# Kernel tuning notes

Measured on AMD Instinct MI355X. Metric: run time of the kernel, lower is better.

Reference implementation:

```python
import jax, jax.numpy as jnp
import numpy as np

B, Q, K, H, DV = 16, 256, 256, 256, 256


def setup_inputs() -> dict:
    key = jax.random.key(0)
    ks = jax.random.split(key, 6)
    return {
        "queries": jax.random.normal(ks[0], (B, Q, H), dtype=jnp.float32),
        "keys": jax.random.normal(ks[1], (B, K, H), dtype=jnp.float32),
        "values": jax.random.normal(ks[2], (B, K, DV), dtype=jnp.float32),
        "W_q": jax.random.normal(ks[3], (H, H), dtype=jnp.float32) / np.sqrt(H),
        "W_k": jax.random.normal(ks[4], (H, H), dtype=jnp.float32) / np.sqrt(H),
        "w_v": jax.random.normal(ks[5], (H,), dtype=jnp.float32) / np.sqrt(H),
    }


def reference(queries, keys, values, W_q, W_k, w_v):
    # Linear projections (nn.Linear: x @ W.T), bias-free
    q = jnp.einsum("bqd,hd->bqh", queries, W_q)  # [B,Q,H]
    k = jnp.einsum("bkd,hd->bkh", keys, W_k)      # [B,K,H]
    # Broadcast add -> tanh -> scalar projection
    features = jnp.tanh(q[:, :, None, :] + k[:, None, :, :])  # [B,Q,K,H]
    scores = jnp.einsum("bqkh,h->bqk", features, w_v)          # [B,Q,K]
    attn = jax.nn.softmax(scores, axis=-1)                      # [B,Q,K]
    return jnp.einsum("bqk,bkv->bqv", attn, values)            # [B,Q,DV]
```

## Files before the change

### kernel.cpp

```cpp
#include <hip/hip_runtime.h>

#define Bn 16
#define Qn 256
#define Kn 256
#define Hn 256
#define DVn 256

constexpr float C2    = 2.8853900817779268f;
constexpr float LOG2E = 1.4426950408889634f;

typedef __attribute__((ext_vector_type(8))) short bf16x8;
typedef __attribute__((ext_vector_type(4))) float f32x4;

__device__ __forceinline__ float fast_exp2(float x) { return __builtin_amdgcn_exp2f(x); }
__device__ __forceinline__ float fast_rcp(float x)  { return __builtin_amdgcn_rcpf(x); }

__device__ __forceinline__ unsigned short f2bf(float x) {
    unsigned u = __float_as_uint(x);
    u += 0x7fffu + ((u >> 16) & 1u);
    return (unsigned short)(u >> 16);
}

__device__ __forceinline__ bf16x8 cvt8(const float* p) {
    float4 x0 = *(const float4*)p;
    float4 x1 = *(const float4*)(p + 4);
    bf16x8 r;
    r[0] = (short)f2bf(x0.x); r[1] = (short)f2bf(x0.y);
    r[2] = (short)f2bf(x0.z); r[3] = (short)f2bf(x0.w);
    r[4] = (short)f2bf(x1.x); r[5] = (short)f2bf(x1.y);
    r[6] = (short)f2bf(x1.z); r[7] = (short)f2bf(x1.w);
    return r;
}

__global__ __launch_bounds__(256)
void proj_mfma_kernel(const float* __restrict__ q, const float* __restrict__ kx,
                      const float* __restrict__ wq, const float* __restrict__ wk,
                      const float* __restrict__ V,
                      float* __restrict__ Eq, unsigned short* __restrict__ Ekb,
                      float* __restrict__ Vp)
{
    const int tid  = threadIdx.x;
    const int wvid = tid >> 6, lane = tid & 63;
    const int bid  = blockIdx.x;
    const int m0   = (bid >> 1) * 16;
    const int n0   = (bid & 1) * 128 + wvid * 32;
    const bool isQ = (m0 < 4096);
    const int r16  = lane & 15, q8 = (lane >> 4) * 8;

    const float* Xrow = (isQ ? q + (size_t)(m0 + r16) * 256
                             : kx + (size_t)(m0 - 4096 + r16) * 256) + q8;
    bf16x8 afr[8];
    #pragma unroll
    for (int s = 0; s < 8; ++s) afr[s] = cvt8(Xrow + s * 32);

    const float* Wbase = isQ ? wq : wk;
    f32x4 acc[2];
    #pragma unroll
    for (int nt = 0; nt < 2; ++nt) {
        const float* Wrow = Wbase + (size_t)(n0 + nt * 16 + r16) * 256 + q8;
        f32x4 c = {0.f, 0.f, 0.f, 0.f};
        #pragma unroll
        for (int s = 0; s < 8; ++s) {
            bf16x8 bfr = cvt8(Wrow + s * 32);
            c = __builtin_amdgcn_mfma_f32_16x16x32_bf16(afr[s], bfr, c, 0, 0, 0);
        }
        acc[nt] = c;
    }
    const int rbase = (lane >> 4) * 4;
    #pragma unroll
    for (int nt = 0; nt < 2; ++nt) {
        const int n = n0 + nt * 16 + r16;
        #pragma unroll
        for (int r = 0; r < 4; ++r) {
            const int m = m0 + rbase + r;
            const float val = fast_exp2(C2 * acc[nt][r]);
            if (isQ) {
                Eq[(size_t)m * 256 + n] = val;
            } else {
                const int kr = m - 4096, b = kr >> 8, kk = kr & 255;
                Ekb[(((size_t)(b * 64 + (n >> 2))) * 256 + kk) * 4 + (n & 3)] = f2bf(val);
            }
        }
    }
    {
        const int p   = bid * 256 + tid;
        const int bk4 = p >> 8, dv = p & 255;
        const int b   = bk4 >> 6, k4 = bk4 & 63;
        const float* src = V + ((size_t)(b * Kn + 4 * k4)) * DVn + dv;
        float4 o;
        o.x = src[0 * DVn]; o.y = src[1 * DVn]; o.z = src[2 * DVn]; o.w = src[3 * DVn];
        *(float4*)(Vp + (size_t)p * 4) = o;
    }
}

__global__ __launch_bounds__(512, 8)
void fused_attn_kernel(const float* __restrict__ Eq, const unsigned short* __restrict__ Ekb,
                       const float* __restrict__ wv, const float* __restrict__ Vp,
                       float* __restrict__ out)
{
    const int b    = blockIdx.y;
    const int q0   = blockIdx.x * 4;
    const int tid  = threadIdx.x;
    const int kk   = tid & 255;
    const int half = tid >> 8;
    const int halfu = __builtin_amdgcn_readfirstlane(half);

    __shared__ __align__(16) float sPart[2][256][4];
    __shared__ __align__(16) float sPv[256 * 4];
    __shared__ float sredM[4][8];
    __shared__ float sredS[4][8];

    const float* eq0 = Eq + (size_t)(b * Qn + q0) * Hn + halfu * 128;
    const float* wv0 = wv + halfu * 128;

    float sc[4] = {0.f, 0.f, 0.f, 0.f};
    const uint2* ekp = (const uint2*)Ekb + (size_t)b * 16384 + (size_t)(halfu * 32) * 256 + kk;
    uint2 e[4];
    #pragma unroll
    for (int g = 0; g < 4; ++g) e[g] = ekp[g * 256];
    for (int it = 0; it < 8; ++it) {
        uint2 en[4];
        if (it < 7) {
            #pragma unroll
            for (int g = 0; g < 4; ++g) en[g] = ekp[(4 * (it + 1) + g) * 256];
        }
        const int h0 = it * 16;
        float ek[16];
        #pragma unroll
        for (int g = 0; g < 4; ++g) {
            ek[4*g+0] = __uint_as_float(e[g].x << 16);
            ek[4*g+1] = __uint_as_float(e[g].x & 0xFFFF0000u);
            ek[4*g+2] = __uint_as_float(e[g].y << 16);
            ek[4*g+3] = __uint_as_float(e[g].y & 0xFFFF0000u);
        }
        #pragma unroll
        for (int g = 0; g < 4; ++g) {
            const float4 wa = *(const float4*)(wv0 + h0 + 4 * g);
            #pragma unroll
            for (int qq = 0; qq < 4; ++qq) {
                const float4 ea = *(const float4*)(eq0 + qq * 256 + h0 + 4 * g);
                float a = sc[qq];
                a = fmaf(wa.x, fast_rcp(fmaf(ea.x, ek[4*g+0], 1.f)), a);
                a = fmaf(wa.y, fast_rcp(fmaf(ea.y, ek[4*g+1], 1.f)), a);
                a = fmaf(wa.z, fast_rcp(fmaf(ea.z, ek[4*g+2], 1.f)), a);
                a = fmaf(wa.w, fast_rcp(fmaf(ea.w, ek[4*g+3], 1.f)), a);
                sc[qq] = a;
            }
        }
        #pragma unroll
        for (int g = 0; g < 4; ++g) e[g] = en[g];
    }

    *(float4*)&sPart[half][kk][0] = make_float4(sc[0], sc[1], sc[2], sc[3]);
    __syncthreads();
    const float4 pa = *(const float4*)&sPart[0][kk][0];
    const float4 pb = *(const float4*)&sPart[1][kk][0];
    float tot[4] = {pa.x + pb.x, pa.y + pb.y, pa.z + pb.z, pa.w + pb.w};

    const int w = tid >> 6, lane = tid & 63;
    #pragma unroll
    for (int qq = 0; qq < 4; ++qq) {
        tot[qq] = -2.0f * tot[qq];
        float mx = tot[qq];
        #pragma unroll
        for (int off = 32; off; off >>= 1) mx = fmaxf(mx, __shfl_xor(mx, off, 64));
        if (lane == 0) sredM[qq][w] = mx;
    }
    __syncthreads();
    float pq[4];
    #pragma unroll
    for (int qq = 0; qq < 4; ++qq) {
        float mx = sredM[qq][0];
        #pragma unroll
        for (int i = 1; i < 8; ++i) mx = fmaxf(mx, sredM[qq][i]);
        pq[qq] = fast_exp2(LOG2E * (tot[qq] - mx));
        float s = pq[qq];
        #pragma unroll
        for (int off = 32; off; off >>= 1) s += __shfl_xor(s, off, 64);
        if (lane == 0) sredS[qq][w] = s;
    }
    if (halfu == 0) *(float4*)&sPv[kk * 4] = make_float4(pq[0], pq[1], pq[2], pq[3]);
    __syncthreads();
    float rinv[4];
    #pragma unroll
    for (int qq = 0; qq < 4; ++qq) {
        float s = sredS[qq][0];
        #pragma unroll
        for (int i = 1; i < 8; ++i) s += sredS[qq][i];
        rinv[qq] = fast_rcp(0.5f * s);
    }

    float acc[4] = {0.f, 0.f, 0.f, 0.f};
    const float4* vp = (const float4*)Vp + (size_t)b * 64 * 256 + (size_t)(halfu * 32) * 256 + kk;
    float4 vv = vp[0];
    for (int k4 = 0; k4 < 32; ++k4) {
        float4 vn;
        if (k4 < 31) vn = vp[(k4 + 1) * 256];
        const int kb = (halfu * 32 + k4) * 4;
        const float vj[4] = {vv.x, vv.y, vv.z, vv.w};
        #pragma unroll
        for (int j = 0; j < 4; ++j) {
            const float4 p4 = *(const float4*)&sPv[(kb + j) * 4];
            acc[0] = fmaf(p4.x, vj[j], acc[0]);
            acc[1] = fmaf(p4.y, vj[j], acc[1]);
            acc[2] = fmaf(p4.z, vj[j], acc[2]);
            acc[3] = fmaf(p4.w, vj[j], acc[3]);
        }
        vv = vn;
    }
    *(float4*)&sPart[half][kk][0] = make_float4(acc[0], acc[1], acc[2], acc[3]);
    __syncthreads();
    {
        const int dv = kk;
        const float4 u0 = *(const float4*)&sPart[0][dv][0];
        const float4 u1 = *(const float4*)&sPart[1][dv][0];
        float a0, a1;
        if (halfu == 0) { a0 = u0.x + u1.x; a1 = u0.y + u1.y; }
        else            { a0 = u0.z + u1.z; a1 = u0.w + u1.w; }
        float* ob = out + (size_t)(b * Qn + q0 + 2 * halfu) * DVn + dv;
        ob[0]   = a0 * rinv[2 * halfu + 0];
        ob[DVn] = a1 * rinv[2 * halfu + 1];
    }
}

extern "C" void kernel_launch(void* const* d_in, const int* in_sizes, int n_in,
                              void* d_out, int out_size, void* d_ws, size_t ws_size,
                              hipStream_t stream) {
    const float* queries = (const float*)d_in[0];
    const float* keys    = (const float*)d_in[1];
    const float* values  = (const float*)d_in[2];
    const float* W_q     = (const float*)d_in[3];
    const float* W_k     = (const float*)d_in[4];
    const float* w_v     = (const float*)d_in[5];
    float* out = (float*)d_out;

    float*          Eq  = (float*)d_ws;
    unsigned short* Ekb = (unsigned short*)(Eq + (size_t)Bn * Qn * Hn);
    float*          Vp  = (float*)(Ekb + (size_t)Bn * Kn * Hn);

    proj_mfma_kernel<<<dim3(1024), 256, 0, stream>>>(queries, keys, W_q, W_k, values,
                                                     Eq, Ekb, Vp);
    fused_attn_kernel<<<dim3(64, 16), 512, 0, stream>>>(Eq, Ekb, w_v, Vp, out);
}
```

Before: 132.8 us.

## Pre-convert inputs and weights to bf16 in separate prep kernel before MFMA projection

Adds a prep kernel that converts queries, keys and both weight matrices to bf16 once and also performs the V repacking. The projection kernel then loads bf16 fragments directly and each block covers all 256 output columns (4 waves x 64), halving the grid. This removes the repeated fp32-to-bf16 conversion of the weight rows in every block and halves how often the X rows are reread. In exchange it adds an extra kernel launch and a round trip of the bf16 copies through global memory.

```diff
diff --git a/kernel.cpp b/kernel.cpp
--- a/kernel.cpp
+++ b/kernel.cpp
@@ -1,4 +1,5 @@
 #include <hip/hip_runtime.h>
+#include <hip/hip_fp16.h>
 
 #define Bn 16
 #define Qn 256
@@ -21,54 +22,78 @@
     return (unsigned short)(u >> 16);
 }
 
-__device__ __forceinline__ bf16x8 cvt8(const float* p) {
-    float4 x0 = *(const float4*)p;
-    float4 x1 = *(const float4*)(p + 4);
-    bf16x8 r;
-    r[0] = (short)f2bf(x0.x); r[1] = (short)f2bf(x0.y);
-    r[2] = (short)f2bf(x0.z); r[3] = (short)f2bf(x0.w);
-    r[4] = (short)f2bf(x1.x); r[5] = (short)f2bf(x1.y);
-    r[6] = (short)f2bf(x1.z); r[7] = (short)f2bf(x1.w);
-    return r;
-}
-
 __global__ __launch_bounds__(256)
-void proj_mfma_kernel(const float* __restrict__ q, const float* __restrict__ kx,
-                      const float* __restrict__ wq, const float* __restrict__ wk,
-                      const float* __restrict__ V,
-                      float* __restrict__ Eq, unsigned short* __restrict__ Ekb,
-                      float* __restrict__ Vp)
+void prep_kernel(const float* __restrict__ q, const float* __restrict__ kx,
+                 const float* __restrict__ wq, const float* __restrict__ wk,
+                 const float* __restrict__ V,
+                 unsigned short* __restrict__ Xb, unsigned short* __restrict__ Wb,
+                 float* __restrict__ Vp)
+{
+    const int g = blockIdx.x * 256 + threadIdx.x;
+    {
+        const float* xs = (g < 131072) ? (q + (size_t)g * 8)
+                                       : (kx + (size_t)(g - 131072) * 8);
+        float4 x0 = *(const float4*)xs;
+        float4 x1 = *(const float4*)(xs + 4);
+        ushort4 o0, o1;
+        o0.x = f2bf(x0.x); o0.y = f2bf(x0.y); o0.z = f2bf(x0.z); o0.w = f2bf(x0.w);
+        o1.x = f2bf(x1.x); o1.y = f2bf(x1.y); o1.z = f2bf(x1.z); o1.w = f2bf(x1.w);
+        *(ushort4*)(Xb + (size_t)g * 8)     = o0;
+        *(ushort4*)(Xb + (size_t)g * 8 + 4) = o1;
+    }
+    if (g < 32768) {
+        const float* ws = (g < 16384) ? (wq + (size_t)g * 4)
+                                      : (wk + (size_t)(g - 16384) * 4);
+        float4 w0 = *(const float4*)ws;
+        ushort4 o;
+        o.x = f2bf(w0.x); o.y = f2bf(w0.y); o.z = f2bf(w0.z); o.w = f2bf(w0.w);
+        *(ushort4*)(Wb + (size_t)g * 4) = o;
+    }
+    {
+        const int p   = g;
+        const int bk4 = p >> 8, dv = p & 255;
+        const int b   = bk4 >> 6, k4 = bk4 & 63;
+        const float* src = V + ((size_t)(b * Kn + 4 * k4)) * DVn + dv;
+        float4 o;
+        o.x = src[0 * DVn]; o.y = src[1 * DVn]; o.z = src[2 * DVn]; o.w = src[3 * DVn];
+        *(float4*)(Vp + (size_t)p * 4) = o;
+    }
+}
+
+__global__ __launch_bounds__(256)
+void proj_mfma_kernel(const unsigned short* __restrict__ Xb,
+                      const unsigned short* __restrict__ Wb,
+                      float* __restrict__ Eq, unsigned short* __restrict__ Ekb)
 {
     const int tid  = threadIdx.x;
     const int wvid = tid >> 6, lane = tid & 63;
-    const int bid  = blockIdx.x;
-    const int m0   = (bid >> 1) * 16;
-    const int n0   = (bid & 1) * 128 + wvid * 32;
+    const int m0   = blockIdx.x * 16;
+    const int n0   = wvid * 64;
     const bool isQ = (m0 < 4096);
     const int r16  = lane & 15, q8 = (lane >> 4) * 8;
 
-    const float* Xrow = (isQ ? q + (size_t)(m0 + r16) * 256
-                             : kx + (size_t)(m0 - 4096 + r16) * 256) + q8;
+    const unsigned short* Xrow  = Xb + (size_t)(m0 + r16) * 256 + q8;
+    const unsigned short* Wbase = Wb + (isQ ? 0 : 65536);
+
     bf16x8 afr[8];
     #pragma unroll
-    for (int s = 0; s < 8; ++s) afr[s] = cvt8(Xrow + s * 32);
-
-    const float* Wbase = isQ ? wq : wk;
-    f32x4 acc[2];
-    #pragma unroll
-    for (int nt = 0; nt < 2; ++nt) {
-        const float* Wrow = Wbase + (size_t)(n0 + nt * 16 + r16) * 256 + q8;
+    for (int s = 0; s < 8; ++s) afr[s] = *(const bf16x8*)(Xrow + s * 32);
+
+    f32x4 acc[4];
+    #pragma unroll
+    for (int nt = 0; nt < 4; ++nt) {
+        const unsigned short* Wrow = Wbase + (size_t)(n0 + nt * 16 + r16) * 256 + q8;
         f32x4 c = {0.f, 0.f, 0.f, 0.f};
         #pragma unroll
         for (int s = 0; s < 8; ++s) {
-            bf16x8 bfr = cvt8(Wrow + s * 32);
+            bf16x8 bfr = *(const bf16x8*)(Wrow + s * 32);
             c = __builtin_amdgcn_mfma_f32_16x16x32_bf16(afr[s], bfr, c, 0, 0, 0);
         }
         acc[nt] = c;
     }
     const int rbase = (lane >> 4) * 4;
     #pragma unroll
-    for (int nt = 0; nt < 2; ++nt) {
+    for (int nt = 0; nt < 4; ++nt) {
         const int n = n0 + nt * 16 + r16;
         #pragma unroll
         for (int r = 0; r < 4; ++r) {
@@ -81,15 +106,6 @@
                 Ekb[(((size_t)(b * 64 + (n >> 2))) * 256 + kk) * 4 + (n & 3)] = f2bf(val);
             }
         }
-    }
-    {
-        const int p   = bid * 256 + tid;
-        const int bk4 = p >> 8, dv = p & 255;
-        const int b   = bk4 >> 6, k4 = bk4 & 63;
-        const float* src = V + ((size_t)(b * Kn + 4 * k4)) * DVn + dv;
-        float4 o;
-        o.x = src[0 * DVn]; o.y = src[1 * DVn]; o.z = src[2 * DVn]; o.w = src[3 * DVn];
-        *(float4*)(Vp + (size_t)p * 4) = o;
     }
 }
 
@@ -237,8 +253,11 @@
     float*          Eq  = (float*)d_ws;
     unsigned short* Ekb = (unsigned short*)(Eq + (size_t)Bn * Qn * Hn);
     float*          Vp  = (float*)(Ekb + (size_t)Bn * Kn * Hn);
-
-    proj_mfma_kernel<<<dim3(1024), 256, 0, stream>>>(queries, keys, W_q, W_k, values,
-                                                     Eq, Ekb, Vp);
+    unsigned short* Xb  = (unsigned short*)(Vp + (size_t)Bn * Kn * DVn);
+    unsigned short* Wb  = Xb + (size_t)2 * Bn * Qn * Hn;
+
+    prep_kernel<<<dim3(1024), 256, 0, stream>>>(queries, keys, W_q, W_k, values,
+                                                Xb, Wb, Vp);
+    proj_mfma_kernel<<<dim3(512), 256, 0, stream>>>(Xb, Wb, Eq, Ekb);
     fused_attn_kernel<<<dim3(64, 16), 512, 0, stream>>>(Eq, Ekb, w_v, Vp, out);
 }
```

After: 127.1 us. 1.05x faster.
